# Kernel tuning notes

Hardware: AMD Instinct MI355X
Metric: run time of the kernel (lower is better)

## Reference

```python
import jax, jax.numpy as jnp
import numpy as np

EPS = 1e-8      # torch CosineSimilarity eps (clamps norms)
GAMMA = 0.5
RANK = 2        # hardcoded in the module; rank-1 = 1 negative per sample


def _cos_dist(a, b):
    # angular distance sqrt(2*(1-cos)) along last dim, torch-style eps on norms
    na = jnp.clip(jnp.linalg.norm(a, axis=-1), EPS)
    nb = jnp.clip(jnp.linalg.norm(b, axis=-1), EPS)
    sim = jnp.sum(a * b, axis=-1) / (na * nb)
    return jnp.sqrt(jnp.maximum(2.0 * (1.0 - sim), 1e-12))


def setup_inputs() -> dict:
    key = jax.random.key(0)
    k1, k2, k3 = jax.random.split(key, 3)
    B, D, V = 4096, 512, 50000
    return {
        "input": jax.random.normal(k1, (B, D), dtype=jnp.float32),
        "target": jax.random.normal(k2, (B, D), dtype=jnp.float32),
        "veclist": jax.random.normal(k3, (V, D), dtype=jnp.float32),
    }


def reference(input, target, veclist):
    B = input.shape[0]
    # distance to the true target per sample: [B]
    d_pos = _cos_dist(input, target)

    # brute-force angular kNN over veclist (replaces the Annoy index):
    # max cosine similarity == min angular distance
    inn = input / jnp.clip(jnp.linalg.norm(input, axis=-1, keepdims=True), EPS)
    vnn = veclist / jnp.clip(jnp.linalg.norm(veclist, axis=-1, keepdims=True), EPS)
    sims = inn @ vnn.T                                # [B, V] -- the big GEMM
    _, top_idx = jax.lax.top_k(sims, RANK)            # [B, 2]

    vec0 = veclist[top_idx[:, 0]]                     # [B, D]
    vec1 = veclist[top_idx[:, 1]]                     # [B, D]
    # skip the neighbor if it is exactly the target vector (original `torch.eq` check)
    eq0 = jnp.all(vec0 == target, axis=-1)            # [B]
    neg = jnp.where(eq0[:, None], vec1, vec0)         # [B, D]

    d_neg = _cos_dist(input, neg)                     # [B]
    # original builds sample_dist of shape [rank]=[2] (gamma_vec bug repeats gamma
    # `rank` times), with both entries identical -> sum of positives = 2*relu(margin)
    margin = GAMMA + d_pos - d_neg                    # [B]
    cost = jnp.sum(RANK * jnp.maximum(margin, 0.0))
    return cost / B
```

## Files before the change

### kernel.cpp

```cpp
#include <hip/hip_runtime.h>
#include <hip/hip_bf16.h>
#include <hip/hip_fp8.h>
#include <math.h>

#define B_ROWS 4096
#define DIMS   512
#define V_ROWS 50000
#define V_PAD  50048
#define NTILES 391
#define NT_VIRT 392
#define MTILES 32
#define NROWS_ALL 54144
#define EPSF   1e-8f
#define QSCALE 64.0f
#define SCALE1 0x7F7F7F7F

typedef float f32x4 __attribute__((ext_vector_type(4)));
typedef int   i32x4 __attribute__((ext_vector_type(4)));
typedef int   i32x8 __attribute__((ext_vector_type(8)));
typedef unsigned long long u64;

__device__ __forceinline__ unsigned int pk4_fp8(float a, float b, float c, float d) {
#if __has_builtin(__builtin_amdgcn_cvt_pk_fp8_f32)
  int w = __builtin_amdgcn_cvt_pk_fp8_f32(a, b, 0, false);
  w = __builtin_amdgcn_cvt_pk_fp8_f32(c, d, w, true);
  return (unsigned int)w;
#else
  __hip_fp8_e4m3 qa(a), qb(b), qc(c), qd(d);
  return (unsigned int)qa.__x | ((unsigned int)qb.__x << 8) |
         ((unsigned int)qc.__x << 16) | ((unsigned int)qd.__x << 24);
#endif
}

__device__ __forceinline__ u64 pack_key2(float v, unsigned int ncol) {
  unsigned int u = __float_as_uint(v);
  unsigned int s = u ^ ((unsigned int)((int)u >> 31) | 0x80000000u);
  return ((u64)s << 32) | ncol;
}
__device__ __forceinline__ int key_col(u64 k) {
  return (int)(~(unsigned int)k);
}
__device__ __forceinline__ void kmerge(u64& k0, u64& k1, u64 a0, u64 a1) {
  bool bt = a0 > k0;
  u64 lo = bt ? k0 : a0;
  u64 hi = bt ? a1 : k1;
  k0 = bt ? a0 : k0;
  k1 = hi > lo ? hi : lo;
}

__global__ __launch_bounds__(256)
void normalize_rows_kernel(const float* __restrict__ vsrc, const float* __restrict__ isrc,
                           unsigned char* __restrict__ vpk, unsigned char* __restrict__ apk) {
  const int l = threadIdx.x & 63;
  const int gw = (blockIdx.x * 256 + threadIdx.x) >> 6;
  const int nw = (gridDim.x * 256) >> 6;
  for (int row = gw; row < NROWS_ALL; row += nw) {
    const float* src;
    unsigned char* dstbase;
    int m;
    if (row < V_PAD) {
      dstbase = vpk; m = row;
      src = (row < V_ROWS) ? (vsrc + (size_t)row * DIMS) : nullptr;
    } else {
      dstbase = apk; m = row - V_PAD;
      src = isrc + (size_t)m * DIMS;
    }
    const int rec = (((( (m >> 7) * 2 + ((m >> 6) & 1) ) * 4 + (l >> 4)) * 4
                      + ((m >> 4) & 3)) * 2 + ((l >> 1) & 1));
    const int off = rec * 1024 + (((l >> 2) & 3) * 16 + (m & 15)) * 16 + (l & 1) * 8;
    if (!src) {
      *(uint2*)&dstbase[off] = make_uint2(0u, 0u);
      continue;
    }
    float4 v0 = ((const float4*)src)[l * 2];
    float4 v1 = ((const float4*)src)[l * 2 + 1];
    float ss = v0.x * v0.x + v0.y * v0.y + v0.z * v0.z + v0.w * v0.w
             + v1.x * v1.x + v1.y * v1.y + v1.z * v1.z + v1.w * v1.w;
    #pragma unroll
    for (int d = 1; d < 64; d <<= 1) ss += __shfl_xor(ss, d);
    float s = QSCALE / fmaxf(sqrtf(ss), EPSF);
    uint2 o;
    o.x = pk4_fp8(v0.x * s, v0.y * s, v0.z * s, v0.w * s);
    o.y = pk4_fp8(v1.x * s, v1.y * s, v1.z * s, v1.w * s);
    *(uint2*)&dstbase[off] = o;
  }
}

__global__ __launch_bounds__(256, 3)
void gemm_top2_kernel(const unsigned char* __restrict__ Apk,
                      const unsigned char* __restrict__ Bpk,
                      ulonglong2* __restrict__ cands) {
  __shared__ __align__(16) ulonglong2 ep[64][32];

  const int bid = blockIdx.x;
  const int xcd = bid & 7;
  const int g   = bid >> 3;
  const int mt  = g & 31;
  const int nt  = xcd * 49 + (g >> 5);
  if (nt >= NTILES) return;
  const int m0 = mt * 128, n0 = nt * 128;

  const int tid = threadIdx.x;
  const int w = tid >> 6, l = tid & 63;
  const int wr = w >> 1, wc = w & 1;
  const int lq = l >> 4, lr = l & 15;

  const unsigned char* aP = Apk + (size_t)(mt * 2 + wr) * 32768 + l * 16;
  const unsigned char* bP = Bpk + (size_t)(nt * 2 + wc) * 32768 + l * 16;

  f32x4 acc[4][4] = {};

  #pragma unroll
  for (int ks = 0; ks < 4; ++ks) {
    i32x8 bf[4], af[4];
    #pragma unroll
    for (int tc = 0; tc < 4; ++tc) {
      i32x4 lo = *(const i32x4*)(bP + tc * 2048);
      i32x4 hi = *(const i32x4*)(bP + tc * 2048 + 1024);
      bf[tc] = __builtin_shufflevector(lo, hi, 0, 1, 2, 3, 4, 5, 6, 7);
    }
    #pragma unroll
    for (int tr = 0; tr < 4; ++tr) {
      i32x4 lo = *(const i32x4*)(aP + tr * 2048);
      i32x4 hi = *(const i32x4*)(aP + tr * 2048 + 1024);
      af[tr] = __builtin_shufflevector(lo, hi, 0, 1, 2, 3, 4, 5, 6, 7);
    }
    __builtin_amdgcn_s_setprio(1);
    #pragma unroll
    for (int tr = 0; tr < 4; ++tr)
      #pragma unroll
      for (int tc = 0; tc < 4; ++tc)
        acc[tr][tc] = __builtin_amdgcn_mfma_scale_f32_16x16x128_f8f6f4(
            af[tr], bf[tc], acc[tr][tc],
            0, 0,
            0, SCALE1,
            0, SCALE1);
    __builtin_amdgcn_s_setprio(0);
    aP += 8192; bP += 8192;
  }

  const int colbase = n0 + wc * 64 + lr;

  if (n0 + 128 > V_ROWS) {
    #pragma unroll
    for (int tc = 0; tc < 4; ++tc) {
      if (colbase + tc * 16 >= V_ROWS) {
        #pragma unroll
        for (int tr = 0; tr < 4; ++tr)
          #pragma unroll
          for (int rg = 0; rg < 4; ++rg) acc[tr][tc][rg] = -INFINITY;
      }
    }
  }
  unsigned int nc[4];
  #pragma unroll
  for (int tc = 0; tc < 4; ++tc) nc[tc] = ~(unsigned int)(colbase + tc * 16);

  #pragma unroll
  for (int p = 0; p < 2; ++p) {
    #pragma unroll
    for (int trh = 0; trh < 2; ++trh) {
      const int tr = p * 2 + trh;
      #pragma unroll
      for (int rg = 0; rg < 4; ++rg) {
        u64 kk[4];
        #pragma unroll
        for (int tc = 0; tc < 4; ++tc)
          kk[tc] = pack_key2(acc[tr][tc][rg], nc[tc]);
        const bool s01 = kk[0] > kk[1];
        u64 a0 = s01 ? kk[0] : kk[1], a1 = s01 ? kk[1] : kk[0];
        const bool s23 = kk[2] > kk[3];
        u64 b0 = s23 ? kk[2] : kk[3], b1 = s23 ? kk[3] : kk[2];
        kmerge(a0, a1, b0, b1);
        const int slot = wr * 32 + trh * 16 + lq * 4 + rg;
        ep[slot][(wc * 16 + lr) ^ (slot & 7)] = make_ulonglong2(a0, a1);
      }
    }
    __syncthreads();
    {
      const int ms = tid >> 2, q = tid & 3;
      u64 k0 = 0, k1 = 0;
      #pragma unroll
      for (int k = 0; k < 8; ++k) {
        ulonglong2 e = ep[ms][(q * 8 + k) ^ (ms & 7)];
        kmerge(k0, k1, e.x, e.y);
      }
      #pragma unroll
      for (int d = 1; d < 4; d <<= 1) {
        u64 o0 = __shfl_xor(k0, d), o1 = __shfl_xor(k1, d);
        kmerge(k0, k1, o0, o1);
      }
      if (q == 0) {
        const int row = (ms >> 5) * 64 + p * 32 + (ms & 31);
        cands[(size_t)nt * B_ROWS + (m0 + row)] = make_ulonglong2(k0, k1);
      }
    }
    __syncthreads();
  }
}

__global__ __launch_bounds__(256)
void finalize_kernel(const float* __restrict__ input, const float* __restrict__ target,
                     const float* __restrict__ veclist, const ulonglong2* __restrict__ cands,
                     float* __restrict__ contrib) {
  const int b = blockIdx.x;
  const int t = threadIdx.x;
  __shared__ ulonglong2 wpair[4];
  __shared__ int sidx[2];
  __shared__ float red[4][7];
  __shared__ int reda[4];

  u64 k0 = 0, k1 = 0;
  for (int nt = t; nt < NTILES; nt += 256) {
    ulonglong2 c = cands[(size_t)nt * B_ROWS + b];
    kmerge(k0, k1, c.x, c.y);
  }
  #pragma unroll
  for (int d = 1; d < 64; d <<= 1) {
    u64 o0 = __shfl_xor(k0, d), o1 = __shfl_xor(k1, d);
    kmerge(k0, k1, o0, o1);
  }
  if ((t & 63) == 0) wpair[t >> 6] = make_ulonglong2(k0, k1);
  __syncthreads();
  if (t == 0) {
    u64 m0k = wpair[0].x, m1k = wpair[0].y;
    for (int wd = 1; wd < 4; ++wd) kmerge(m0k, m1k, wpair[wd].x, wpair[wd].y);
    sidx[0] = key_col(m0k);
    sidx[1] = key_col(m1k);
  }
  __syncthreads();
  const int idx0 = sidx[0], idx1 = sidx[1];

  const float2* xin = (const float2*)(input  + (size_t)b * DIMS);
  const float2* xtg = (const float2*)(target + (size_t)b * DIMS);
  const float2* xv0 = (const float2*)(veclist + (size_t)idx0 * DIMS);
  const float2* xv1 = (const float2*)(veclist + (size_t)idx1 * DIMS);
  float2 xi = xin[t], tg = xtg[t], a0 = xv0[t], a1 = xv1[t];
  float s[7];
  s[0] = xi.x * xi.x + xi.y * xi.y;
  s[1] = tg.x * tg.x + tg.y * tg.y;
  s[2] = xi.x * tg.x + xi.y * tg.y;
  s[3] = a0.x * a0.x + a0.y * a0.y;
  s[4] = xi.x * a0.x + xi.y * a0.y;
  s[5] = a1.x * a1.x + a1.y * a1.y;
  s[6] = xi.x * a1.x + xi.y * a1.y;
  bool eq = (a0.x == tg.x) && (a0.y == tg.y);
  int weq = __all(eq);
  #pragma unroll
  for (int k = 0; k < 7; ++k)
    #pragma unroll
    for (int d = 1; d < 64; d <<= 1) s[k] += __shfl_xor(s[k], d);
  if ((t & 63) == 0) {
    #pragma unroll
    for (int k = 0; k < 7; ++k) red[t >> 6][k] = s[k];
    reda[t >> 6] = weq;
  }
  __syncthreads();
  if (t == 0) {
    float r[7];
    #pragma unroll
    for (int k = 0; k < 7; ++k)
      r[k] = red[0][k] + red[1][k] + red[2][k] + red[3][k];
    bool eq0 = reda[0] && reda[1] && reda[2] && reda[3];
    float na  = fmaxf(sqrtf(r[0]), EPSF);
    float ntg = fmaxf(sqrtf(r[1]), EPSF);
    float simp = r[2] / (na * ntg);
    float d_pos = sqrtf(fmaxf(2.0f * (1.0f - simp), 1e-12f));
    float nn = eq0 ? fmaxf(sqrtf(r[5]), EPSF) : fmaxf(sqrtf(r[3]), EPSF);
    float dn = eq0 ? r[6] : r[4];
    float simn = dn / (na * nn);
    float d_neg = sqrtf(fmaxf(2.0f * (1.0f - simn), 1e-12f));
    float margin = 0.5f + d_pos - d_neg;
    contrib[b] = 2.0f * fmaxf(margin, 0.0f) * (1.0f / (float)B_ROWS);
  }
}

__global__ __launch_bounds__(256)
void reduce_kernel(const float* __restrict__ contrib, float* __restrict__ out) {
  const int t = threadIdx.x;
  __shared__ float wsum[4];
  float s = 0.0f;
  for (int i = t; i < B_ROWS; i += 256) s += contrib[i];
  #pragma unroll
  for (int d = 1; d < 64; d <<= 1) s += __shfl_xor(s, d);
  if ((t & 63) == 0) wsum[t >> 6] = s;
  __syncthreads();
  if (t == 0) out[0] = wsum[0] + wsum[1] + wsum[2] + wsum[3];
}

extern "C" void kernel_launch(void* const* d_in, const int* in_sizes, int n_in,
                              void* d_out, int out_size, void* d_ws, size_t ws_size,
                              hipStream_t stream) {
  const float* input   = (const float*)d_in[0];
  const float* target  = (const float*)d_in[1];
  const float* veclist = (const float*)d_in[2];
  float* out = (float*)d_out;
  char* ws = (char*)d_ws;
  unsigned char* vpk = (unsigned char*)ws;
  unsigned char* apk = (unsigned char*)(ws + 25624576);
  ulonglong2* cands = (ulonglong2*)(ws + 27721728);
  float* contrib = (float*)(ws + 53411840);

  normalize_rows_kernel<<<4096, 256, 0, stream>>>(veclist, input, vpk, apk);
  gemm_top2_kernel<<<NT_VIRT * MTILES, 256, 0, stream>>>(apk, vpk, cands);
  finalize_kernel<<<B_ROWS, 256, 0, stream>>>(input, target, veclist, cands, contrib);
  reduce_kernel<<<1, 256, 0, stream>>>(contrib, out);
}
```

Measured before the change: 342.3 us.

## Stage fp8 packing through LDS and batch eight rows per finalize block

The normalize kernel now processes 64-row chunks per block. It stages the fp8-packed output in a 32 KB shared buffer with an XOR swizzle, then writes it out as contiguous 16-byte stores instead of scattered 8-byte stores. The finalize kernel handles eight batch rows per block: it merges top-2 candidates across 32 threads per row, then computes the dot products one wave per two rows with float4 loads. This removes the block-wide shared reductions. The aim is to cut uncoalesced writes and per-block overhead in the pre- and post-GEMM stages, at the cost of more shared memory and lower parallelism in the packing kernel.

```diff
diff --git a/kernel.cpp b/kernel.cpp
--- a/kernel.cpp
+++ b/kernel.cpp
@@ -10,7 +10,8 @@
 #define NTILES 391
 #define NT_VIRT 392
 #define MTILES 32
-#define NROWS_ALL 54144
+#define VCHUNKS 782
+#define ACHUNKS 64
 #define EPSF   1e-8f
 #define QSCALE 64.0f
 #define SCALE1 0x7F7F7F7F
@@ -49,40 +50,50 @@
 }
 
 __global__ __launch_bounds__(256)
-void normalize_rows_kernel(const float* __restrict__ vsrc, const float* __restrict__ isrc,
+void normalize_pack_kernel(const float* __restrict__ vsrc, const float* __restrict__ isrc,
                            unsigned char* __restrict__ vpk, unsigned char* __restrict__ apk) {
-  const int l = threadIdx.x & 63;
-  const int gw = (blockIdx.x * 256 + threadIdx.x) >> 6;
-  const int nw = (gridDim.x * 256) >> 6;
-  for (int row = gw; row < NROWS_ALL; row += nw) {
-    const float* src;
-    unsigned char* dstbase;
-    int m;
-    if (row < V_PAD) {
-      dstbase = vpk; m = row;
-      src = (row < V_ROWS) ? (vsrc + (size_t)row * DIMS) : nullptr;
-    } else {
-      dstbase = apk; m = row - V_PAD;
-      src = isrc + (size_t)m * DIMS;
-    }
-    const int rec = (((( (m >> 7) * 2 + ((m >> 6) & 1) ) * 4 + (l >> 4)) * 4
-                      + ((m >> 4) & 3)) * 2 + ((l >> 1) & 1));
-    const int off = rec * 1024 + (((l >> 2) & 3) * 16 + (m & 15)) * 16 + (l & 1) * 8;
-    if (!src) {
-      *(uint2*)&dstbase[off] = make_uint2(0u, 0u);
-      continue;
-    }
-    float4 v0 = ((const float4*)src)[l * 2];
-    float4 v1 = ((const float4*)src)[l * 2 + 1];
-    float ss = v0.x * v0.x + v0.y * v0.y + v0.z * v0.z + v0.w * v0.w
-             + v1.x * v1.x + v1.y * v1.y + v1.z * v1.z + v1.w * v1.w;
-    #pragma unroll
-    for (int d = 1; d < 64; d <<= 1) ss += __shfl_xor(ss, d);
-    float s = QSCALE / fmaxf(sqrtf(ss), EPSF);
-    uint2 o;
-    o.x = pk4_fp8(v0.x * s, v0.y * s, v0.z * s, v0.w * s);
-    o.y = pk4_fp8(v1.x * s, v1.y * s, v1.z * s, v1.w * s);
-    *(uint2*)&dstbase[off] = o;
+  __shared__ __align__(16) unsigned char st[32768];
+
+  const int chunk = blockIdx.x;
+  const bool isA = chunk >= VCHUNKS;
+  const int row0 = (isA ? (chunk - VCHUNKS) : chunk) * 64;
+  const float* const src0 = isA ? isrc : vsrc;
+  unsigned char* const dst = (isA ? apk : vpk) +
+      (size_t)(isA ? (chunk - VCHUNKS) : chunk) * 32768;
+
+  const int tid = threadIdx.x;
+  const int w = tid >> 6, l = tid & 63;
+  const int ks = l >> 4, lq = (l >> 2) & 3, khalf = (l >> 1) & 1, by = l & 1;
+  const int key = (ks << 1) | khalf;
+
+  #pragma unroll
+  for (int i = 0; i < 16; ++i) {
+    const int mloc = w * 16 + i;
+    const int m = row0 + mloc;
+    uint2 o = make_uint2(0u, 0u);
+    if (isA || m < V_ROWS) {
+      const float* src = src0 + (size_t)m * DIMS;
+      float4 v0 = ((const float4*)src)[l * 2];
+      float4 v1 = ((const float4*)src)[l * 2 + 1];
+      float ss = v0.x * v0.x + v0.y * v0.y + v0.z * v0.z + v0.w * v0.w
+               + v1.x * v1.x + v1.y * v1.y + v1.z * v1.z + v1.w * v1.w;
+      #pragma unroll
+      for (int d = 1; d < 64; d <<= 1) ss += __shfl_xor(ss, d);
+      float s = QSCALE / fmaxf(sqrtf(ss), EPSF);
+      o.x = pk4_fp8(v0.x * s, v0.y * s, v0.z * s, v0.w * s);
+      o.y = pk4_fp8(v1.x * s, v1.y * s, v1.z * s, v1.w * s);
+    }
+    const int rec = ks * 8 + w * 2 + khalf;
+    const int slot = (lq * 16 + (mloc & 15)) ^ key;
+    *(uint2*)&st[rec * 1024 + slot * 16 + by * 8] = o;
+  }
+  __syncthreads();
+  #pragma unroll
+  for (int it = 0; it < 8; ++it) {
+    const int c = it * 256 + tid;
+    const int r = c >> 6, s = c & 63;
+    const int k2 = ((r >> 3) << 1) | (r & 1);
+    *(uint4*)&dst[c * 16] = *(const uint4*)&st[r * 1024 + (s ^ k2) * 16];
   }
 }
 
@@ -203,75 +214,73 @@
 void finalize_kernel(const float* __restrict__ input, const float* __restrict__ target,
                      const float* __restrict__ veclist, const ulonglong2* __restrict__ cands,
                      float* __restrict__ contrib) {
-  const int b = blockIdx.x;
+  __shared__ ulonglong2 lp[8][33];
+  __shared__ int sidx[8][2];
+
+  const int blk = blockIdx.x;
+  const int b0 = blk * 8;
   const int t = threadIdx.x;
-  __shared__ ulonglong2 wpair[4];
-  __shared__ int sidx[2];
-  __shared__ float red[4][7];
-  __shared__ int reda[4];
+  const int i = t & 7, j = t >> 3;
 
   u64 k0 = 0, k1 = 0;
-  for (int nt = t; nt < NTILES; nt += 256) {
-    ulonglong2 c = cands[(size_t)nt * B_ROWS + b];
+  for (int nt = j; nt < NTILES; nt += 32) {
+    ulonglong2 c = cands[(size_t)nt * B_ROWS + b0 + i];
     kmerge(k0, k1, c.x, c.y);
   }
-  #pragma unroll
-  for (int d = 1; d < 64; d <<= 1) {
-    u64 o0 = __shfl_xor(k0, d), o1 = __shfl_xor(k1, d);
-    kmerge(k0, k1, o0, o1);
-  }
-  if ((t & 63) == 0) wpair[t >> 6] = make_ulonglong2(k0, k1);
+  lp[i][j] = make_ulonglong2(k0, k1);
   __syncthreads();
-  if (t == 0) {
-    u64 m0k = wpair[0].x, m1k = wpair[0].y;
-    for (int wd = 1; wd < 4; ++wd) kmerge(m0k, m1k, wpair[wd].x, wpair[wd].y);
-    sidx[0] = key_col(m0k);
-    sidx[1] = key_col(m1k);
+  if (t < 8) {
+    u64 m0 = lp[t][0].x, m1 = lp[t][0].y;
+    #pragma unroll
+    for (int jj = 1; jj < 32; ++jj) kmerge(m0, m1, lp[t][jj].x, lp[t][jj].y);
+    sidx[t][0] = key_col(m0);
+    sidx[t][1] = key_col(m1);
   }
   __syncthreads();
-  const int idx0 = sidx[0], idx1 = sidx[1];
-
-  const float2* xin = (const float2*)(input  + (size_t)b * DIMS);
-  const float2* xtg = (const float2*)(target + (size_t)b * DIMS);
-  const float2* xv0 = (const float2*)(veclist + (size_t)idx0 * DIMS);
-  const float2* xv1 = (const float2*)(veclist + (size_t)idx1 * DIMS);
-  float2 xi = xin[t], tg = xtg[t], a0 = xv0[t], a1 = xv1[t];
-  float s[7];
-  s[0] = xi.x * xi.x + xi.y * xi.y;
-  s[1] = tg.x * tg.x + tg.y * tg.y;
-  s[2] = xi.x * tg.x + xi.y * tg.y;
-  s[3] = a0.x * a0.x + a0.y * a0.y;
-  s[4] = xi.x * a0.x + xi.y * a0.y;
-  s[5] = a1.x * a1.x + a1.y * a1.y;
-  s[6] = xi.x * a1.x + xi.y * a1.y;
-  bool eq = (a0.x == tg.x) && (a0.y == tg.y);
-  int weq = __all(eq);
-  #pragma unroll
-  for (int k = 0; k < 7; ++k)
-    #pragma unroll
-    for (int d = 1; d < 64; d <<= 1) s[k] += __shfl_xor(s[k], d);
-  if ((t & 63) == 0) {
-    #pragma unroll
-    for (int k = 0; k < 7; ++k) red[t >> 6][k] = s[k];
-    reda[t >> 6] = weq;
-  }
-  __syncthreads();
-  if (t == 0) {
-    float r[7];
+
+  const int w = t >> 6, l = t & 63;
+  #pragma unroll
+  for (int rr = 0; rr < 2; ++rr) {
+    const int i2 = w * 2 + rr;
+    const int b = b0 + i2;
+    const int idx0 = sidx[i2][0], idx1 = sidx[i2][1];
+    const float4* xin = (const float4*)(input  + (size_t)b * DIMS);
+    const float4* xtg = (const float4*)(target + (size_t)b * DIMS);
+    const float4* xv0 = (const float4*)(veclist + (size_t)idx0 * DIMS);
+    const float4* xv1 = (const float4*)(veclist + (size_t)idx1 * DIMS);
+    float s[7] = {0, 0, 0, 0, 0, 0, 0};
+    bool eq = true;
+    #pragma unroll
+    for (int c = 0; c < 2; ++c) {
+      float4 xi = xin[l + c * 64], tg = xtg[l + c * 64];
+      float4 a0 = xv0[l + c * 64], a1 = xv1[l + c * 64];
+      s[0] += xi.x * xi.x + xi.y * xi.y + xi.z * xi.z + xi.w * xi.w;
+      s[1] += tg.x * tg.x + tg.y * tg.y + tg.z * tg.z + tg.w * tg.w;
+      s[2] += xi.x * tg.x + xi.y * tg.y + xi.z * tg.z + xi.w * tg.w;
+      s[3] += a0.x * a0.x + a0.y * a0.y + a0.z * a0.z + a0.w * a0.w;
+      s[4] += xi.x * a0.x + xi.y * a0.y + xi.z * a0.z + xi.w * a0.w;
+      s[5] += a1.x * a1.x + a1.y * a1.y + a1.z * a1.z + a1.w * a1.w;
+      s[6] += xi.x * a1.x + xi.y * a1.y + xi.z * a1.z + xi.w * a1.w;
+      eq = eq && (a0.x == tg.x) && (a0.y == tg.y) && (a0.z == tg.z) && (a0.w == tg.w);
+    }
+    int weq = __all(eq);
     #pragma unroll
     for (int k = 0; k < 7; ++k)
-      r[k] = red[0][k] + red[1][k] + red[2][k] + red[3][k];
-    bool eq0 = reda[0] && reda[1] && reda[2] && reda[3];
-    float na  = fmaxf(sqrtf(r[0]), EPSF);
-    float ntg = fmaxf(sqrtf(r[1]), EPSF);
-    float simp = r[2] / (na * ntg);
-    float d_pos = sqrtf(fmaxf(2.0f * (1.0f - simp), 1e-12f));
-    float nn = eq0 ? fmaxf(sqrtf(r[5]), EPSF) : fmaxf(sqrtf(r[3]), EPSF);
-    float dn = eq0 ? r[6] : r[4];
-    float simn = dn / (na * nn);
-    float d_neg = sqrtf(fmaxf(2.0f * (1.0f - simn), 1e-12f));
-    float margin = 0.5f + d_pos - d_neg;
-    contrib[b] = 2.0f * fmaxf(margin, 0.0f) * (1.0f / (float)B_ROWS);
+      #pragma unroll
+      for (int d = 1; d < 64; d <<= 1) s[k] += __shfl_xor(s[k], d);
+    if (l == 0) {
+      bool eq0 = (weq != 0);
+      float na  = fmaxf(sqrtf(s[0]), EPSF);
+      float ntg = fmaxf(sqrtf(s[1]), EPSF);
+      float simp = s[2] / (na * ntg);
+      float d_pos = sqrtf(fmaxf(2.0f * (1.0f - simp), 1e-12f));
+      float nn = eq0 ? fmaxf(sqrtf(s[5]), EPSF) : fmaxf(sqrtf(s[3]), EPSF);
+      float dn = eq0 ? s[6] : s[4];
+      float simn = dn / (na * nn);
+      float d_neg = sqrtf(fmaxf(2.0f * (1.0f - simn), 1e-12f));
+      float margin = 0.5f + d_pos - d_neg;
+      contrib[b] = 2.0f * fmaxf(margin, 0.0f) * (1.0f / (float)B_ROWS);
+    }
   }
 }
 
@@ -301,8 +310,8 @@
   ulonglong2* cands = (ulonglong2*)(ws + 27721728);
   float* contrib = (float*)(ws + 53411840);
 
-  normalize_rows_kernel<<<4096, 256, 0, stream>>>(veclist, input, vpk, apk);
+  normalize_pack_kernel<<<VCHUNKS + ACHUNKS, 256, 0, stream>>>(veclist, input, vpk, apk);
   gemm_top2_kernel<<<NT_VIRT * MTILES, 256, 0, stream>>>(apk, vpk, cands);
-  finalize_kernel<<<B_ROWS, 256, 0, stream>>>(input, target, veclist, cands, contrib);
+  finalize_kernel<<<B_ROWS / 8, 256, 0, stream>>>(input, target, veclist, cands, contrib);
   reduce_kernel<<<1, 256, 0, stream>>>(contrib, out);
 }
```

New measurement: 320.4 us. 1.07x faster.
